# Performance work log

Hardware: AMD Instinct MI355X
Metric: run time of the kernel (lower is better)

## Reference

```python
import jax, jax.numpy as jnp
import numpy as np

TAU = 2.0      # LIF membrane time constant
ALPHA = 4.0    # spikingjelly surrogate.Sigmoid default alpha
EPS = 1e-5     # BatchNorm eps
HEADS = 8

@jax.custom_vjp
def heaviside(x):
    return (x >= 0).astype(x.dtype)

def _hv_fwd(x):
    return (x >= 0).astype(x.dtype), x

def _hv_bwd(x, g):
    s = jax.nn.sigmoid(ALPHA * x)
    return (g * ALPHA * s * (1.0 - s),)

heaviside.defvjp(_hv_fwd, _hv_bwd)

def lif(x, vth=1.0):
    # multi-step LIF, decay_input=True, v_reset=0 (hard reset), detach_reset=True
    def step(v, xt):
        v = v + (xt - v) / TAU
        s = heaviside(v - vth)
        v = v * (1.0 - jax.lax.stop_gradient(s))
        return v, s
    _, spikes = jax.lax.scan(step, jnp.zeros_like(x[0]), x)
    return spikes

def bn(x, gamma, beta, mean, var):
    # x: [T,B,C,N]; eval-mode BatchNorm1d over channel axis 2
    inv = gamma * jax.lax.rsqrt(var + EPS)
    return x * inv[None, None, :, None] + (beta - mean * inv)[None, None, :, None]

def conv1x1(x, w):
    # x: [T,B,C,N], w: [Cout,Cin] (Conv1d kernel_size=1)
    return jnp.einsum('tbcn,dc->tbdn', x, w)

def setup_inputs():
    key = jax.random.key(0)
    ks = jax.random.split(key, 24)
    T, B, C, H, W = 4, 16, 512, 32, 32
    scale = 1.0 / np.sqrt(C)
    d = {}
    d['x'] = jax.random.normal(ks[0], (T, B, C, H, W), jnp.float32)
    def bn_params(i):
        g = 1.0 + 0.1 * jax.random.normal(ks[i], (C,), jnp.float32)
        b = 0.1 * jax.random.normal(ks[i + 1], (C,), jnp.float32)
        m = 0.1 * jax.random.normal(ks[i + 2], (C,), jnp.float32)
        v = jax.random.uniform(ks[i + 3], (C,), jnp.float32, 0.5, 1.5)
        return g, b, m, v
    d['q_w'] = scale * jax.random.normal(ks[1], (C, C), jnp.float32)
    d['q_gamma'], d['q_beta'], d['q_mean'], d['q_var'] = bn_params(2)
    d['k_w'] = scale * jax.random.normal(ks[6], (C, C), jnp.float32)
    d['k_gamma'], d['k_beta'], d['k_mean'], d['k_var'] = bn_params(7)
    d['proj_w'] = scale * jax.random.normal(ks[11], (C, C), jnp.float32)
    d['proj_b'] = 0.01 * jax.random.normal(ks[12], (C,), jnp.float32)
    d['p_gamma'], d['p_beta'], d['p_mean'], d['p_var'] = bn_params(13)
    return d

def reference(x, q_w, q_gamma, q_beta, q_mean, q_var,
              k_w, k_gamma, k_beta, k_mean, k_var,
              proj_w, proj_b, p_gamma, p_beta, p_mean, p_var):
    T, B, C, H, W = x.shape
    N = H * W
    Dh = C // HEADS
    xs = lif(x).reshape(T, B, C, N)                    # shortcut_lif then flatten(3)
    q = lif(bn(conv1x1(xs, q_w), q_gamma, q_beta, q_mean, q_var))
    k = lif(bn(conv1x1(xs, k_w), k_gamma, k_beta, k_mean, k_var))
    qh = q.reshape(T, B, HEADS, Dh, N).sum(axis=3, keepdims=True)  # [T,B,h,1,N]
    attn = lif(qh, vth=0.5)
    kh = k.reshape(T, B, HEADS, Dh, N)
    y = (attn * kh).reshape(T, B, C, N)
    y = bn(conv1x1(y, proj_w) + proj_b[None, None, :, None],
           p_gamma, p_beta, p_mean, p_var)
    return y.reshape(T, B, C, H, W), attn
```

## Files before the change

kernel.cpp:

```cpp
#include <hip/hip_runtime.h>

typedef unsigned short u16;
typedef unsigned int u32;
typedef float f32x4 __attribute__((ext_vector_type(4)));
typedef short s16x8 __attribute__((ext_vector_type(8)));

#define T_ 4
#define B_ 16
#define C_ 512
#define N_ 1024
#define TB_ 64
#define YSZ 33554432

__device__ __forceinline__ u16 f2bf(float f) {
  u32 u = __float_as_uint(f);
  u32 r = u + 0x7FFFu + ((u >> 16) & 1u);
  return (u16)(r >> 16);
}
__device__ __forceinline__ float bf2f(u16 h) { return __uint_as_float(((u32)h) << 16); }

__device__ __forceinline__ void async16(const void* g, void* l) {
  __builtin_amdgcn_global_load_lds((const __attribute__((address_space(1))) void*)g,
                                   (__attribute__((address_space(3))) void*)l, 16, 0, 0);
}

__global__ void prep_kernel(const float* __restrict__ qw, const float* __restrict__ kw,
                            const float* __restrict__ pw,
                            const float* __restrict__ qg, const float* __restrict__ qb,
                            const float* __restrict__ qm, const float* __restrict__ qv,
                            const float* __restrict__ kg, const float* __restrict__ kb,
                            const float* __restrict__ km, const float* __restrict__ kv,
                            const float* __restrict__ pg, const float* __restrict__ pbt,
                            const float* __restrict__ pm, const float* __restrict__ pv,
                            u16* __restrict__ whlq, u16* __restrict__ whlk,
                            u16* __restrict__ pwb, float* __restrict__ consts) {
  int blk = blockIdx.x, tid = threadIdx.x;
  if (blk < 512) {
    int d = blk;
    for (int c = tid; c < 512; c += 256) {
      float w = qw[d * 512 + c];
      u16 hi = f2bf(w);
      whlq[d * 1024 + c] = hi;
      whlq[d * 1024 + 512 + c] = f2bf(w - bf2f(hi));
      w = kw[d * 512 + c];
      hi = f2bf(w);
      whlk[d * 1024 + c] = hi;
      whlk[d * 1024 + 512 + c] = f2bf(w - bf2f(hi));
      pwb[d * 512 + c] = f2bf(pw[d * 512 + c]);
    }
  } else {
    for (int c = tid; c < 512; c += 256) {
      float inv = qg[c] / sqrtf(qv[c] + 1e-5f);
      consts[c] = inv; consts[512 + c] = qb[c] - qm[c] * inv;
      inv = kg[c] / sqrtf(kv[c] + 1e-5f);
      consts[1024 + c] = inv; consts[1536 + c] = kb[c] - km[c] * inv;
      inv = pg[c] / sqrtf(pv[c] + 1e-5f);
      consts[2048 + c] = inv; consts[2560 + c] = pbt[c] - pm[c] * inv;
    }
  }
}

__global__ __launch_bounds__(256) void lifx_kernel(const float* __restrict__ x,
                                                   u16* __restrict__ xs) {
  int b = blockIdx.z;
  int cbase = blockIdx.y * 64, nbase = blockIdx.x * 64;
  int tid = threadIdx.x;
  int c_l = tid >> 6, n_l = tid & 63;
  __shared__ __align__(16) u16 tile[64 * 72];
  float v[16];
#pragma unroll
  for (int i = 0; i < 16; ++i) v[i] = 0.f;
  for (int t = 0; t < 4; ++t) {
    const float* xp = x + ((size_t)(t * 16 + b) * 512 + cbase + c_l * 16) * 1024 + nbase + n_l;
#pragma unroll
    for (int i = 0; i < 16; ++i) {
      float xv = xp[(size_t)i * 1024];
      float vn = v[i] + 0.5f * (xv - v[i]);
      bool s = vn >= 1.0f;
      tile[n_l * 72 + c_l * 16 + i] = s ? 0x3F80 : 0;
      v[i] = s ? 0.f : vn;
    }
    __syncthreads();
    u16* yb = xs + ((size_t)(t * 16 + b) * 1024 + nbase) * 512 + cbase;
#pragma unroll
    for (int e = 0; e < 2; ++e) {
      int chunk = tid * 2 + e;
      int n = chunk >> 3, c0 = (chunk & 7) * 8;
      *(uint4*)&yb[(size_t)n * 512 + c0] = *(const uint4*)&tile[n * 72 + c0];
    }
    __syncthreads();
  }
}

__global__ __launch_bounds__(256) void qpass_kernel(const float* __restrict__ conv,
                                                    const float* __restrict__ consts,
                                                    float* __restrict__ dout) {
  int b = blockIdx.z, h = blockIdx.y;
  int n = blockIdx.x * 256 + threadIdx.x;
  const float* qinv = consts;
  const float* qbias = consts + 512;
  float qh[4] = {0.f, 0.f, 0.f, 0.f};
  for (int dh = 0; dh < 64; ++dh) {
    int c = h * 64 + dh;
    float iv = qinv[c], ib = qbias[c];
    float v = 0.f;
#pragma unroll
    for (int t = 0; t < 4; ++t) {
      float cv = conv[((size_t)(t * 16 + b) * 512 + c) * 1024 + n];
      float bnv = cv * iv + ib;
      float vn = v + 0.5f * (bnv - v);
      bool s = vn >= 1.0f;
      qh[t] += s ? 1.f : 0.f;
      v = s ? 0.f : vn;
    }
  }
  float va = 0.f;
#pragma unroll
  for (int t = 0; t < 4; ++t) {
    float vn = va + 0.5f * (qh[t] - va);
    bool s = vn >= 0.5f;
    dout[(size_t)YSZ + ((size_t)(t * 16 + b) * 8 + h) * 1024 + n] = s ? 1.f : 0.f;
    va = s ? 0.f : vn;
  }
}

__global__ __launch_bounds__(256) void kpass_kernel(const float* __restrict__ conv,
                                                    const float* __restrict__ consts,
                                                    const float* __restrict__ dout,
                                                    u16* __restrict__ y) {
  int b = blockIdx.z, h = blockIdx.y;
  int cbase = h * 64, nbase = blockIdx.x * 64;
  int tid = threadIdx.x;
  int c_l = tid >> 6, n_l = tid & 63;
  const float* kinv = consts + 1024;
  const float* kbias = consts + 1536;
  __shared__ __align__(16) u16 tile[64 * 72];
  float v[16], iv[16], ib[16];
#pragma unroll
  for (int i = 0; i < 16; ++i) {
    v[i] = 0.f;
    iv[i] = kinv[cbase + c_l * 16 + i];
    ib[i] = kbias[cbase + c_l * 16 + i];
  }
  for (int t = 0; t < 4; ++t) {
    float a = dout[(size_t)YSZ + ((size_t)(t * 16 + b) * 8 + h) * 1024 + nbase + n_l];
    const float* cp = conv + ((size_t)(t * 16 + b) * 512 + cbase + c_l * 16) * 1024 + nbase + n_l;
#pragma unroll
    for (int i = 0; i < 16; ++i) {
      float bnv = cp[(size_t)i * 1024] * iv[i] + ib[i];
      float vn = v[i] + 0.5f * (bnv - v[i]);
      bool s = vn >= 1.0f;
      tile[n_l * 72 + c_l * 16 + i] = (s && a != 0.f) ? 0x3F80 : 0;
      v[i] = s ? 0.f : vn;
    }
    __syncthreads();
    u16* yb = y + ((size_t)(t * 16 + b) * 1024 + nbase) * 512 + cbase;
#pragma unroll
    for (int e = 0; e < 2; ++e) {
      int chunk = tid * 2 + e;
      int n = chunk >> 3, c0 = (chunk & 7) * 8;
      *(uint4*)&yb[(size_t)n * 512 + c0] = *(const uint4*)&tile[n * 72 + c0];
    }
    __syncthreads();
  }
}

template <int MODE>
__global__ __launch_bounds__(256, 3) void gemm_kernel(
    const u16* __restrict__ A, int lda, int K, const u16* __restrict__ Bbase,
    float* __restrict__ outC, float* __restrict__ outP,
    const float* __restrict__ projb, const float* __restrict__ consts) {
  const int tid = threadIdx.x;
  const int lane = tid & 63, w = tid >> 6;
  const int wm = w >> 1, wn = w & 1;
  const int quad = lane >> 4, l16 = lane & 15;
  const int tb = blockIdx.z;
  const int m_blk = blockIdx.y * 128, n_blk = blockIdx.x * 128;
  const int srow = lane >> 3;
  const int scol = (((lane & 7) ^ srow) & 7) * 8;
  __shared__ __align__(16) u16 As[128 * 64];
  __shared__ __align__(16) u16 Bs[128 * 64];
  f32x4 acc[4][4];
  const f32x4 zero = {0.f, 0.f, 0.f, 0.f};
#pragma unroll
  for (int i = 0; i < 4; ++i)
#pragma unroll
    for (int j = 0; j < 4; ++j) acc[i][j] = zero;
  const u16* Bt = Bbase + (size_t)tb * (N_ * C_);
  const int rxor = l16 & 7;

  for (int k0 = 0; k0 < K; k0 += 64) {
    int ck0 = k0 & 511;
#pragma unroll
    for (int i = 0; i < 4; ++i) {
      int r = i * 32 + w * 8 + srow;
      async16(A + (size_t)(m_blk + r) * lda + k0 + scol, &As[(i * 32 + w * 8) * 64]);
      async16(Bt + (size_t)(n_blk + r) * 512 + ck0 + scol, &Bs[(i * 32 + w * 8) * 64]);
    }
    __syncthreads();
#pragma unroll
    for (int kk = 0; kk < 2; ++kk) {
      s16x8 af[4], bf[4];
      const int slot = ((kk * 4 + quad) ^ rxor) * 8;
#pragma unroll
      for (int ti = 0; ti < 4; ++ti)
        af[ti] = *(const s16x8*)&As[(wm * 64 + ti * 16 + l16) * 64 + slot];
#pragma unroll
      for (int tj = 0; tj < 4; ++tj)
        bf[tj] = *(const s16x8*)&Bs[(wn * 64 + tj * 16 + l16) * 64 + slot];
#pragma unroll
      for (int ti = 0; ti < 4; ++ti)
#pragma unroll
        for (int tj = 0; tj < 4; ++tj)
          acc[ti][tj] = __builtin_amdgcn_mfma_f32_16x16x32_bf16(af[ti], bf[tj], acc[ti][tj], 0, 0, 0);
    }
    __syncthreads();
  }

  if (MODE == 0) {
    float* o = outC + (size_t)tb * (C_ * N_);
#pragma unroll
    for (int ti = 0; ti < 4; ++ti) {
      int row0 = m_blk + wm * 64 + ti * 16 + quad * 4;
#pragma unroll
      for (int tj = 0; tj < 4; ++tj) {
        int col = n_blk + wn * 64 + tj * 16 + l16;
#pragma unroll
        for (int r = 0; r < 4; ++r) o[(size_t)(row0 + r) * N_ + col] = acc[ti][tj][r];
      }
    }
  } else {
    const float* pinv = consts + 2048;
    const float* pb2 = consts + 2560;
    float* o = outP + (size_t)tb * (C_ * N_);
#pragma unroll
    for (int ti = 0; ti < 4; ++ti) {
      int row0 = m_blk + wm * 64 + ti * 16 + quad * 4;
#pragma unroll
      for (int r = 0; r < 4; ++r) {
        int row = row0 + r;
        float bi = projb[row], piv = pinv[row], pbi = pb2[row];
#pragma unroll
        for (int tj = 0; tj < 4; ++tj) {
          int col = n_blk + wn * 64 + tj * 16 + l16;
          o[(size_t)row * N_ + col] = (acc[ti][tj][r] + bi) * piv + pbi;
        }
      }
    }
  }
}

extern "C" void kernel_launch(void* const* d_in, const int* in_sizes, int n_in,
                              void* d_out, int out_size, void* d_ws, size_t ws_size,
                              hipStream_t stream) {
  const float* x   = (const float*)d_in[0];
  const float* qw  = (const float*)d_in[1];
  const float* qg  = (const float*)d_in[2];
  const float* qb  = (const float*)d_in[3];
  const float* qm  = (const float*)d_in[4];
  const float* qv  = (const float*)d_in[5];
  const float* kw  = (const float*)d_in[6];
  const float* kg  = (const float*)d_in[7];
  const float* kb  = (const float*)d_in[8];
  const float* km  = (const float*)d_in[9];
  const float* kv  = (const float*)d_in[10];
  const float* pw  = (const float*)d_in[11];
  const float* pb  = (const float*)d_in[12];
  const float* pg  = (const float*)d_in[13];
  const float* pbt = (const float*)d_in[14];
  const float* pm  = (const float*)d_in[15];
  const float* pv  = (const float*)d_in[16];
  float* out = (float*)d_out;
  char* ws = (char*)d_ws;

  u16* xs       = (u16*)ws;
  float* conv   = (float*)(ws + 67108864);
  u16* whlq     = (u16*)(ws + 201326592);
  u16* whlk     = (u16*)(ws + 202375168);
  u16* pwb      = (u16*)(ws + 203423744);
  float* consts = (float*)(ws + 203948032);

  prep_kernel<<<513, 256, 0, stream>>>(qw, kw, pw, qg, qb, qm, qv, kg, kb, km, kv,
                                       pg, pbt, pm, pv, whlq, whlk, pwb, consts);
  lifx_kernel<<<dim3(16, 8, 16), 256, 0, stream>>>(x, xs);
  gemm_kernel<0><<<dim3(8, 4, 64), 256, 0, stream>>>(whlq, 1024, 1024, xs, conv,
                                                     nullptr, nullptr, nullptr);
  qpass_kernel<<<dim3(4, 8, 16), 256, 0, stream>>>(conv, consts, out);
  gemm_kernel<0><<<dim3(8, 4, 64), 256, 0, stream>>>(whlk, 1024, 1024, xs, conv,
                                                     nullptr, nullptr, nullptr);
  kpass_kernel<<<dim3(16, 8, 16), 256, 0, stream>>>(conv, consts, out, xs);
  gemm_kernel<1><<<dim3(8, 4, 64), 256, 0, stream>>>(pwb, 512, 512, xs, nullptr, out,
                                                     pb, consts);
}
```

Baseline: 483.9 us.

## Fuse Q/K GEMMs with BN+LIF epilogues, looping timesteps inside each block

```diff
diff --git a/kernel.cpp b/kernel.cpp
--- a/kernel.cpp
+++ b/kernel.cpp
@@ -9,7 +9,6 @@
 #define B_ 16
 #define C_ 512
 #define N_ 1024
-#define TB_ 64
 #define YSZ 33554432
 
 __device__ __forceinline__ u16 f2bf(float f) {
@@ -92,84 +91,206 @@
   }
 }
 
-__global__ __launch_bounds__(256) void qpass_kernel(const float* __restrict__ conv,
-                                                    const float* __restrict__ consts,
-                                                    float* __restrict__ dout) {
-  int b = blockIdx.z, h = blockIdx.y;
-  int n = blockIdx.x * 256 + threadIdx.x;
-  const float* qinv = consts;
-  const float* qbias = consts + 512;
-  float qh[4] = {0.f, 0.f, 0.f, 0.f};
-  for (int dh = 0; dh < 64; ++dh) {
-    int c = h * 64 + dh;
-    float iv = qinv[c], ib = qbias[c];
-    float v = 0.f;
-#pragma unroll
-    for (int t = 0; t < 4; ++t) {
-      float cv = conv[((size_t)(t * 16 + b) * 512 + c) * 1024 + n];
-      float bnv = cv * iv + ib;
-      float vn = v + 0.5f * (bnv - v);
-      bool s = vn >= 1.0f;
-      qh[t] += s ? 1.f : 0.f;
-      v = s ? 0.f : vn;
-    }
-  }
-  float va = 0.f;
-#pragma unroll
+__global__ __launch_bounds__(256, 2) void gemm_q_kernel(
+    const u16* __restrict__ A, const u16* __restrict__ Bbase,
+    const float* __restrict__ consts, float* __restrict__ dout) {
+  const int tid = threadIdx.x;
+  const int lane = tid & 63, w = tid >> 6;
+  const int wm = w >> 1, wn = w & 1;
+  const int quad = lane >> 4, l16 = lane & 15;
+  const int b = blockIdx.z;
+  const int m_blk = blockIdx.y * 128, n_blk = blockIdx.x * 128;
+  const int srow = lane >> 3;
+  const int scol = (((lane & 7) ^ srow) & 7) * 8;
+  __shared__ __align__(16) u16 As[128 * 64];
+  __shared__ __align__(16) u16 Bs[128 * 64];
+  const int rxor = l16 & 7;
+  float v[64];
+#pragma unroll
+  for (int i = 0; i < 64; ++i) v[i] = 0.f;
+  float va[4] = {0.f, 0.f, 0.f, 0.f};
+
   for (int t = 0; t < 4; ++t) {
-    float vn = va + 0.5f * (qh[t] - va);
-    bool s = vn >= 0.5f;
-    dout[(size_t)YSZ + ((size_t)(t * 16 + b) * 8 + h) * 1024 + n] = s ? 1.f : 0.f;
-    va = s ? 0.f : vn;
-  }
-}
-
-__global__ __launch_bounds__(256) void kpass_kernel(const float* __restrict__ conv,
-                                                    const float* __restrict__ consts,
-                                                    const float* __restrict__ dout,
-                                                    u16* __restrict__ y) {
-  int b = blockIdx.z, h = blockIdx.y;
-  int cbase = h * 64, nbase = blockIdx.x * 64;
-  int tid = threadIdx.x;
-  int c_l = tid >> 6, n_l = tid & 63;
-  const float* kinv = consts + 1024;
-  const float* kbias = consts + 1536;
-  __shared__ __align__(16) u16 tile[64 * 72];
-  float v[16], iv[16], ib[16];
-#pragma unroll
-  for (int i = 0; i < 16; ++i) {
-    v[i] = 0.f;
-    iv[i] = kinv[cbase + c_l * 16 + i];
-    ib[i] = kbias[cbase + c_l * 16 + i];
-  }
+    f32x4 acc[4][4];
+    const f32x4 zero = {0.f, 0.f, 0.f, 0.f};
+#pragma unroll
+    for (int i = 0; i < 4; ++i)
+#pragma unroll
+      for (int j = 0; j < 4; ++j) acc[i][j] = zero;
+    const u16* Bt = Bbase + (size_t)(t * 16 + b) * (N_ * C_);
+
+    for (int k0 = 0; k0 < 1024; k0 += 64) {
+      int ck0 = k0 & 511;
+#pragma unroll
+      for (int i = 0; i < 4; ++i) {
+        int r = i * 32 + w * 8 + srow;
+        async16(A + (size_t)(m_blk + r) * 1024 + k0 + scol, &As[(i * 32 + w * 8) * 64]);
+        async16(Bt + (size_t)(n_blk + r) * 512 + ck0 + scol, &Bs[(i * 32 + w * 8) * 64]);
+      }
+      __syncthreads();
+#pragma unroll
+      for (int kk = 0; kk < 2; ++kk) {
+        s16x8 af[4], bf[4];
+        const int slot = ((kk * 4 + quad) ^ rxor) * 8;
+#pragma unroll
+        for (int ti = 0; ti < 4; ++ti)
+          af[ti] = *(const s16x8*)&As[(wm * 64 + ti * 16 + l16) * 64 + slot];
+#pragma unroll
+        for (int tj = 0; tj < 4; ++tj)
+          bf[tj] = *(const s16x8*)&Bs[(wn * 64 + tj * 16 + l16) * 64 + slot];
+#pragma unroll
+        for (int ti = 0; ti < 4; ++ti)
+#pragma unroll
+          for (int tj = 0; tj < 4; ++tj)
+            acc[ti][tj] = __builtin_amdgcn_mfma_f32_16x16x32_bf16(af[ti], bf[tj], acc[ti][tj], 0, 0, 0);
+      }
+      __syncthreads();
+    }
+
+    float qp[4] = {0.f, 0.f, 0.f, 0.f};
+#pragma unroll
+    for (int ti = 0; ti < 4; ++ti) {
+#pragma unroll
+      for (int r = 0; r < 4; ++r) {
+        int row = m_blk + wm * 64 + ti * 16 + quad * 4 + r;
+        float iv = consts[row], ib = consts[512 + row];
+#pragma unroll
+        for (int tj = 0; tj < 4; ++tj) {
+          float bnv = acc[ti][tj][r] * iv + ib;
+          float vv = v[(ti * 4 + tj) * 4 + r];
+          float vn = vv + 0.5f * (bnv - vv);
+          bool s = vn >= 1.0f;
+          v[(ti * 4 + tj) * 4 + r] = s ? 0.f : vn;
+          qp[tj] += s ? 1.f : 0.f;
+        }
+      }
+    }
+    int h = (m_blk >> 6) + wm;
+#pragma unroll
+    for (int tj = 0; tj < 4; ++tj) {
+      float q = qp[tj];
+      q += __shfl_xor(q, 16, 64);
+      q += __shfl_xor(q, 32, 64);
+      float vn = va[tj] + 0.5f * (q - va[tj]);
+      bool s = vn >= 0.5f;
+      va[tj] = s ? 0.f : vn;
+      if (quad == 0) {
+        int col = n_blk + wn * 64 + tj * 16 + l16;
+        dout[(size_t)YSZ + ((size_t)(t * 16 + b) * 8 + h) * 1024 + col] = s ? 1.f : 0.f;
+      }
+    }
+  }
+}
+
+__global__ __launch_bounds__(256, 2) void gemm_k_kernel(
+    const u16* __restrict__ A, const u16* __restrict__ Bbase,
+    const float* __restrict__ consts, const float* __restrict__ dout,
+    u16* __restrict__ y) {
+  const int tid = threadIdx.x;
+  const int lane = tid & 63, w = tid >> 6;
+  const int wm = w >> 1, wn = w & 1;
+  const int quad = lane >> 4, l16 = lane & 15;
+  const int b = blockIdx.z;
+  const int m_blk = blockIdx.y * 128, n_blk = blockIdx.x * 128;
+  const int srow = lane >> 3;
+  const int scol = (((lane & 7) ^ srow) & 7) * 8;
+  __shared__ __align__(16) u16 smem[128 * 132];
+  u16* As = smem;
+  u16* Bs = smem + 128 * 64;
+  u16* Ys = smem;
+  const int rxor = l16 & 7;
+  float v[64];
+#pragma unroll
+  for (int i = 0; i < 64; ++i) v[i] = 0.f;
+
   for (int t = 0; t < 4; ++t) {
-    float a = dout[(size_t)YSZ + ((size_t)(t * 16 + b) * 8 + h) * 1024 + nbase + n_l];
-    const float* cp = conv + ((size_t)(t * 16 + b) * 512 + cbase + c_l * 16) * 1024 + nbase + n_l;
-#pragma unroll
-    for (int i = 0; i < 16; ++i) {
-      float bnv = cp[(size_t)i * 1024] * iv[i] + ib[i];
-      float vn = v[i] + 0.5f * (bnv - v[i]);
-      bool s = vn >= 1.0f;
-      tile[n_l * 72 + c_l * 16 + i] = (s && a != 0.f) ? 0x3F80 : 0;
-      v[i] = s ? 0.f : vn;
-    }
-    __syncthreads();
-    u16* yb = y + ((size_t)(t * 16 + b) * 1024 + nbase) * 512 + cbase;
-#pragma unroll
-    for (int e = 0; e < 2; ++e) {
-      int chunk = tid * 2 + e;
-      int n = chunk >> 3, c0 = (chunk & 7) * 8;
-      *(uint4*)&yb[(size_t)n * 512 + c0] = *(const uint4*)&tile[n * 72 + c0];
-    }
-    __syncthreads();
-  }
-}
-
-template <int MODE>
-__global__ __launch_bounds__(256, 3) void gemm_kernel(
-    const u16* __restrict__ A, int lda, int K, const u16* __restrict__ Bbase,
-    float* __restrict__ outC, float* __restrict__ outP,
-    const float* __restrict__ projb, const float* __restrict__ consts) {
+    f32x4 acc[4][4];
+    const f32x4 zero = {0.f, 0.f, 0.f, 0.f};
+#pragma unroll
+    for (int i = 0; i < 4; ++i)
+#pragma unroll
+      for (int j = 0; j < 4; ++j) acc[i][j] = zero;
+    const u16* Bt = Bbase + (size_t)(t * 16 + b) * (N_ * C_);
+
+    for (int k0 = 0; k0 < 1024; k0 += 64) {
+      int ck0 = k0 & 511;
+#pragma unroll
+      for (int i = 0; i < 4; ++i) {
+        int r = i * 32 + w * 8 + srow;
+        async16(A + (size_t)(m_blk + r) * 1024 + k0 + scol, &As[(i * 32 + w * 8) * 64]);
+        async16(Bt + (size_t)(n_blk + r) * 512 + ck0 + scol, &Bs[(i * 32 + w * 8) * 64]);
+      }
+      __syncthreads();
+#pragma unroll
+      for (int kk = 0; kk < 2; ++kk) {
+        s16x8 af[4], bf[4];
+        const int slot = ((kk * 4 + quad) ^ rxor) * 8;
+#pragma unroll
+        for (int ti = 0; ti < 4; ++ti)
+          af[ti] = *(const s16x8*)&As[(wm * 64 + ti * 16 + l16) * 64 + slot];
+#pragma unroll
+        for (int tj = 0; tj < 4; ++tj)
+          bf[tj] = *(const s16x8*)&Bs[(wn * 64 + tj * 16 + l16) * 64 + slot];
+#pragma unroll
+        for (int ti = 0; ti < 4; ++ti)
+#pragma unroll
+          for (int tj = 0; tj < 4; ++tj)
+            acc[ti][tj] = __builtin_amdgcn_mfma_f32_16x16x32_bf16(af[ti], bf[tj], acc[ti][tj], 0, 0, 0);
+      }
+      __syncthreads();
+    }
+
+    int h = (m_blk >> 6) + wm;
+    float at[4];
+#pragma unroll
+    for (int tj = 0; tj < 4; ++tj) {
+      int col = n_blk + wn * 64 + tj * 16 + l16;
+      at[tj] = dout[(size_t)YSZ + ((size_t)(t * 16 + b) * 8 + h) * 1024 + col];
+    }
+
+#pragma unroll
+    for (int ti = 0; ti < 4; ++ti) {
+      u16 pk[4][4];
+#pragma unroll
+      for (int r = 0; r < 4; ++r) {
+        int row = m_blk + wm * 64 + ti * 16 + quad * 4 + r;
+        float iv = consts[1024 + row], ib = consts[1536 + row];
+#pragma unroll
+        for (int tj = 0; tj < 4; ++tj) {
+          float bnv = acc[ti][tj][r] * iv + ib;
+          float vv = v[(ti * 4 + tj) * 4 + r];
+          float vn = vv + 0.5f * (bnv - vv);
+          bool s = vn >= 1.0f;
+          v[(ti * 4 + tj) * 4 + r] = s ? 0.f : vn;
+          pk[tj][r] = (s && at[tj] != 0.f) ? 0x3F80 : 0;
+        }
+      }
+#pragma unroll
+      for (int tj = 0; tj < 4; ++tj) {
+        int n_loc = wn * 64 + tj * 16 + l16;
+        int c_loc = wm * 64 + ti * 16 + quad * 4;
+        u32 lo = (u32)pk[tj][0] | ((u32)pk[tj][1] << 16);
+        u32 hi = (u32)pk[tj][2] | ((u32)pk[tj][3] << 16);
+        uint2 pv2; pv2.x = lo; pv2.y = hi;
+        *(uint2*)&Ys[n_loc * 132 + c_loc] = pv2;
+      }
+    }
+    __syncthreads();
+    u16* yb = y + ((size_t)(t * 16 + b) * 1024 + n_blk) * 512 + m_blk;
+#pragma unroll
+    for (int p = 0; p < 8; ++p) {
+      int idx = p * 256 + tid;
+      int rown = idx >> 4, ch = (idx & 15) * 8;
+      *(uint4*)&yb[(size_t)rown * 512 + ch] = *(const uint4*)&Ys[rown * 132 + ch];
+    }
+    __syncthreads();
+  }
+}
+
+__global__ __launch_bounds__(256, 3) void gemm_proj_kernel(
+    const u16* __restrict__ A, const u16* __restrict__ Bbase,
+    float* __restrict__ outP, const float* __restrict__ projb,
+    const float* __restrict__ consts) {
   const int tid = threadIdx.x;
   const int lane = tid & 63, w = tid >> 6;
   const int wm = w >> 1, wn = w & 1;
@@ -189,13 +310,12 @@
   const u16* Bt = Bbase + (size_t)tb * (N_ * C_);
   const int rxor = l16 & 7;
 
-  for (int k0 = 0; k0 < K; k0 += 64) {
-    int ck0 = k0 & 511;
+  for (int k0 = 0; k0 < 512; k0 += 64) {
 #pragma unroll
     for (int i = 0; i < 4; ++i) {
       int r = i * 32 + w * 8 + srow;
-      async16(A + (size_t)(m_blk + r) * lda + k0 + scol, &As[(i * 32 + w * 8) * 64]);
-      async16(Bt + (size_t)(n_blk + r) * 512 + ck0 + scol, &Bs[(i * 32 + w * 8) * 64]);
+      async16(A + (size_t)(m_blk + r) * 512 + k0 + scol, &As[(i * 32 + w * 8) * 64]);
+      async16(Bt + (size_t)(n_blk + r) * 512 + k0 + scol, &Bs[(i * 32 + w * 8) * 64]);
     }
     __syncthreads();
 #pragma unroll
@@ -217,34 +337,20 @@
     __syncthreads();
   }
 
-  if (MODE == 0) {
-    float* o = outC + (size_t)tb * (C_ * N_);
-#pragma unroll
-    for (int ti = 0; ti < 4; ++ti) {
-      int row0 = m_blk + wm * 64 + ti * 16 + quad * 4;
+  const float* pinv = consts + 2048;
+  const float* pb2 = consts + 2560;
+  float* o = outP + (size_t)tb * (C_ * N_);
+#pragma unroll
+  for (int ti = 0; ti < 4; ++ti) {
+    int row0 = m_blk + wm * 64 + ti * 16 + quad * 4;
+#pragma unroll
+    for (int r = 0; r < 4; ++r) {
+      int row = row0 + r;
+      float bi = projb[row], piv = pinv[row], pbi = pb2[row];
 #pragma unroll
       for (int tj = 0; tj < 4; ++tj) {
         int col = n_blk + wn * 64 + tj * 16 + l16;
-#pragma unroll
-        for (int r = 0; r < 4; ++r) o[(size_t)(row0 + r) * N_ + col] = acc[ti][tj][r];
-      }
-    }
-  } else {
-    const float* pinv = consts + 2048;
-    const float* pb2 = consts + 2560;
-    float* o = outP + (size_t)tb * (C_ * N_);
-#pragma unroll
-    for (int ti = 0; ti < 4; ++ti) {
-      int row0 = m_blk + wm * 64 + ti * 16 + quad * 4;
-#pragma unroll
-      for (int r = 0; r < 4; ++r) {
-        int row = row0 + r;
-        float bi = projb[row], piv = pinv[row], pbi = pb2[row];
-#pragma unroll
-        for (int tj = 0; tj < 4; ++tj) {
-          int col = n_blk + wn * 64 + tj * 16 + l16;
-          o[(size_t)row * N_ + col] = (acc[ti][tj][r] + bi) * piv + pbi;
-        }
+        o[(size_t)row * N_ + col] = (acc[ti][tj][r] + bi) * piv + pbi;
       }
     }
   }
@@ -274,7 +380,7 @@
   char* ws = (char*)d_ws;
 
   u16* xs       = (u16*)ws;
-  float* conv   = (float*)(ws + 67108864);
+  u16* y2       = (u16*)(ws + 67108864);
   u16* whlq     = (u16*)(ws + 201326592);
   u16* whlk     = (u16*)(ws + 202375168);
   u16* pwb      = (u16*)(ws + 203423744);
@@ -283,12 +389,7 @@
   prep_kernel<<<513, 256, 0, stream>>>(qw, kw, pw, qg, qb, qm, qv, kg, kb, km, kv,
                                        pg, pbt, pm, pv, whlq, whlk, pwb, consts);
   lifx_kernel<<<dim3(16, 8, 16), 256, 0, stream>>>(x, xs);
-  gemm_kernel<0><<<dim3(8, 4, 64), 256, 0, stream>>>(whlq, 1024, 1024, xs, conv,
-                                                     nullptr, nullptr, nullptr);
-  qpass_kernel<<<dim3(4, 8, 16), 256, 0, stream>>>(conv, consts, out);
-  gemm_kernel<0><<<dim3(8, 4, 64), 256, 0, stream>>>(whlk, 1024, 1024, xs, conv,
-                                                     nullptr, nullptr, nullptr);
-  kpass_kernel<<<dim3(16, 8, 16), 256, 0, stream>>>(conv, consts, out, xs);
-  gemm_kernel<1><<<dim3(8, 4, 64), 256, 0, stream>>>(pwb, 512, 512, xs, nullptr, out,
-                                                     pb, consts);
-}
+  gemm_q_kernel<<<dim3(8, 4, 16), 256, 0, stream>>>(whlq, xs, consts, out);
+  gemm_k_kernel<<<dim3(8, 4, 16), 256, 0, stream>>>(whlk, xs, consts, out, y2);
+  gemm_proj_kernel<<<dim3(8, 4, 64), 256, 0, stream>>>(pwb, y2, out, pb, consts);
+}
```

New measurement: 452.7 us. 6.4% less time.
